# Performance work log

Measured on AMD Instinct MI355X. Metric: run time of the kernel, lower is better.

## Reference

```python
import jax, jax.numpy as jnp
import numpy as np

B, N = 4, 8192
MODEL_DIM, FEAT, HEADS, DIM, SIZE = 512, 64, 8, 3, 32
BN_EPS = 1e-5


def setup_inputs() -> dict:
    key = jax.random.key(0)
    ks = jax.random.split(key, 8)
    return {
        "input": jax.random.normal(ks[0], (B, MODEL_DIM, N), jnp.float32),
        "orig_pcd": jax.random.uniform(ks[1], (B, 3, N), jnp.float32, minval=-1.0, maxval=1.0),
        "conv_w": jax.random.normal(ks[2], (HEADS * (FEAT + 3), MODEL_DIM), jnp.float32) * (MODEL_DIM ** -0.5),
        "key_gamma": jax.random.normal(ks[3], (HEADS * 3,), jnp.float32) * 0.1,
        "key_beta": jnp.zeros((HEADS * 3,), jnp.float32),
        "val_gamma": jnp.ones((HEADS * FEAT,), jnp.float32),
        "val_beta": jnp.zeros((HEADS * FEAT,), jnp.float32),
        "proj": jax.random.normal(ks[4], (HEADS, DIM, 3), jnp.float32) * 0.5,
    }


def _bn(x, gamma, beta):
    # train-mode BatchNorm1d: normalize each channel over (batch, length); x: [B, C, N]
    mu = jnp.mean(x, axis=(0, 2), keepdims=True)
    var = jnp.var(x, axis=(0, 2), keepdims=True)
    xhat = (x - mu) * jax.lax.rsqrt(var + BN_EPS)
    return xhat * gamma[None, :, None] + beta[None, :, None]


def _splat(lattice, values):
    # lattice: [B, H, DIM, N] in (-1, 1); values: [B, H*FEAT, N]
    # DifferentiablePositions: map (-1,1) -> continuous grid coords in [0, SIZE-1]
    c = (lattice + 1.0) * 0.5 * (SIZE - 1)
    f = jnp.clip(jnp.floor(c), 0, SIZE - 2).astype(jnp.int32)   # base corner
    r = c - f.astype(c.dtype)                                    # local coord, [B,H,DIM,N]
    vals = values.reshape(B, HEADS, FEAT, N)
    data = jnp.moveaxis(vals, 2, -1)                             # [B,H,N,FEAT]
    strides = jnp.array([SIZE ** (DIM - 1 - d) for d in range(DIM)], jnp.int32)
    ncells = SIZE ** DIM
    bh = jnp.arange(B)[:, None] * HEADS + jnp.arange(HEADS)[None, :]  # [B,H]
    z = jnp.zeros((B * HEADS * ncells, FEAT), jnp.float32)
    # trilinear splat: scatter-add into the 2^DIM surrounding lattice cells
    for corner in range(2 ** DIM):
        bits = jnp.array([(corner >> (DIM - 1 - d)) & 1 for d in range(DIM)], jnp.int32)
        bits4 = bits[None, None, :, None]
        idx = f + bits4                                           # [B,H,DIM,N]
        w = jnp.prod(jnp.where(bits4 == 1, r, 1.0 - r), axis=2)   # [B,H,N]
        flat = jnp.sum(idx * strides[None, None, :, None], axis=2)  # [B,H,N]
        gid = (bh[:, :, None] * ncells + flat).reshape(-1)        # [B*H*N]
        z = z.at[gid].add((data * w[..., None]).reshape(-1, FEAT))
    return z.reshape(B, HEADS, ncells, FEAT).transpose(0, 1, 3, 2).reshape((B, HEADS, FEAT) + (SIZE,) * DIM)


def reference(input, orig_pcd, conv_w, key_gamma, key_beta, val_gamma, val_beta, proj):
    # 1x1 conv == channel GEMM: [B, H*(FEAT+3), N]
    kv = jnp.einsum('om,bmn->bon', conv_w, input)
    keys_res = _bn(kv[:, :HEADS * 3], key_gamma, key_beta)        # [B, H*3, N]
    values = _bn(kv[:, HEADS * 3:], val_gamma, val_beta)          # [B, H*FEAT, N]
    # per-head learned 3D->DIM projection of (pcd + predicted offset)
    pts = orig_pcd[:, None] + keys_res.reshape(B, HEADS, 3, N)    # [B,H,3,N]
    keys = jnp.einsum('hdk,bhkn->bhdn', proj, pts)                # [B,H,DIM,N]
    lattice = jnp.tanh(keys)
    z = _splat(lattice, values)                                   # [B,H,FEAT,S,S,S]
    occ = (jnp.abs(z) > 1e-9).sum().astype(jnp.float32) / (B * FEAT * HEADS)
    return z, occ, jnp.mean(keys), jnp.var(keys)
```

## Files before the change

kernel.cpp:

```cpp
#include <hip/hip_runtime.h>

#define B_     4
#define N_     8192
#define MD_    512
#define OC_    536
#define HEADS_ 8
#define FEAT_  64
#define NC_    32768
#define ZTOT_  67108864ll
#define NPTS_  262144
#define NKEYS_ 786432.0f

typedef __bf16 bf16x8 __attribute__((ext_vector_type(8)));
typedef float  f32x4  __attribute__((ext_vector_type(4)));

__device__ __forceinline__ unsigned short f2bf(float f) {
  unsigned int u = __float_as_uint(f);
  u = (u + 0x7FFFu + ((u >> 16) & 1u)) >> 16;
  return (unsigned short)u;
}
__device__ __forceinline__ float bf2f(unsigned short s) {
  return __uint_as_float(((unsigned)s) << 16);
}

__global__ __launch_bounds__(256) void convw_kernel(const float* __restrict__ W,
                                                    unsigned short* __restrict__ Wbf) {
  int i = (blockIdx.x * 256 + threadIdx.x) * 4;
  float4 v = *(const float4*)&W[24 * 512 + i];
  ushort4 o;
  o.x = f2bf(v.x); o.y = f2bf(v.y); o.z = f2bf(v.z); o.w = f2bf(v.w);
  *(ushort4*)&Wbf[i] = o;
}

__global__ __launch_bounds__(256) void convxt_kernel(const float* __restrict__ X,
                                                     unsigned short* __restrict__ Xt) {
  const int n0 = blockIdx.x * 64;
  const int k0 = blockIdx.y * 64;
  const int b  = blockIdx.z;
  __shared__ float T[64][65];
  const int t = threadIdx.x;
#pragma unroll
  for (int i = 0; i < 16; ++i) {
    int idx = t + i * 256;
    int kk = idx >> 6, nn = idx & 63;
    T[kk][nn] = X[((size_t)b * MD_ + k0 + kk) * N_ + n0 + nn];
  }
  __syncthreads();
  const int sub = t & 7;
  const int nb  = t >> 3;
#pragma unroll
  for (int i = 0; i < 2; ++i) {
    int nn = nb + i * 32;
    ushort4 o0, o1;
    o0.x = f2bf(T[sub * 8 + 0][nn]); o0.y = f2bf(T[sub * 8 + 1][nn]);
    o0.z = f2bf(T[sub * 8 + 2][nn]); o0.w = f2bf(T[sub * 8 + 3][nn]);
    o1.x = f2bf(T[sub * 8 + 4][nn]); o1.y = f2bf(T[sub * 8 + 5][nn]);
    o1.z = f2bf(T[sub * 8 + 6][nn]); o1.w = f2bf(T[sub * 8 + 7][nn]);
    unsigned short* dst = Xt + ((size_t)b * N_ + n0 + nn) * MD_ + k0 + sub * 8;
    *(ushort4*)dst = o0;
    *(ushort4*)(dst + 4) = o1;
  }
}

__global__ __launch_bounds__(256) void gemm_keys(const float* __restrict__ W,
                                                 const float* __restrict__ X,
                                                 float* __restrict__ kvk,
                                                 float* __restrict__ ssum,
                                                 float* __restrict__ s2sum) {
  const int n0 = blockIdx.x * 256;
  const int b  = blockIdx.y;
  __shared__ float Wt[32][26];
  __shared__ float In[32][260];
  const int t  = threadIdx.x;
  const int cg = t & 63;
  const int rb = (t >> 6) * 6;
  float acc[6][4];
#pragma unroll
  for (int r = 0; r < 6; ++r)
#pragma unroll
    for (int c = 0; c < 4; ++c) acc[r][c] = 0.f;
  const float* Xb = X + (size_t)b * MD_ * N_;
  for (int k0 = 0; k0 < MD_; k0 += 32) {
#pragma unroll
    for (int i = 0; i < 3; ++i) {
      int idx = t * 3 + i;
      int m = idx % 24, k = idx / 24;
      Wt[k][m] = W[(size_t)m * MD_ + k0 + k];
    }
#pragma unroll
    for (int i = 0; i < 8; ++i) {
      int slot = t + i * 256;
      int k = slot >> 6, n4 = slot & 63;
      float4 v = *(const float4*)(Xb + (size_t)(k0 + k) * N_ + n0 + n4 * 4);
      *(float4*)&In[k][n4 * 4] = v;
    }
    __syncthreads();
#pragma unroll
    for (int k = 0; k < 32; ++k) {
      float4 bv = *(const float4*)&In[k][cg * 4];
#pragma unroll
      for (int r = 0; r < 6; ++r) {
        float a = Wt[k][rb + r];
        acc[r][0] = fmaf(a, bv.x, acc[r][0]);
        acc[r][1] = fmaf(a, bv.y, acc[r][1]);
        acc[r][2] = fmaf(a, bv.z, acc[r][2]);
        acc[r][3] = fmaf(a, bv.w, acc[r][3]);
      }
    }
    __syncthreads();
  }
#pragma unroll
  for (int r = 0; r < 6; ++r) {
    float* dst = kvk + ((size_t)b * 24 + rb + r) * N_ + n0 + cg * 4;
    *(float4*)dst = *(float4*)&acc[r][0];
    float s = acc[r][0] + acc[r][1] + acc[r][2] + acc[r][3];
    float s2 = acc[r][0]*acc[r][0] + acc[r][1]*acc[r][1] +
               acc[r][2]*acc[r][2] + acc[r][3]*acc[r][3];
#pragma unroll
    for (int off = 32; off; off >>= 1) {
      s  += __shfl_down(s, off);
      s2 += __shfl_down(s2, off);
    }
    if (cg == 0) { atomicAdd(&ssum[rb + r], s); atomicAdd(&s2sum[rb + r], s2); }
  }
}

__global__ __launch_bounds__(256) void gemm_mfma(const unsigned short* __restrict__ Wbf,
                                                 const unsigned short* __restrict__ Xt,
                                                 unsigned short* __restrict__ valsbf,
                                                 float* __restrict__ ssum,
                                                 float* __restrict__ s2sum) {
  const int m0 = blockIdx.x * 128;
  const int n0 = blockIdx.y * 128;
  const int b  = blockIdx.z;
  __shared__ __align__(16) unsigned short Al[128][72];
  __shared__ __align__(16) unsigned short Bl[128][72];
  const int t = threadIdx.x;
  const int lane = t & 63, wave = t >> 6;
  const int wm = wave >> 1, wn = wave & 1;
  f32x4 acc[4][4];
#pragma unroll
  for (int mi = 0; mi < 4; ++mi)
#pragma unroll
    for (int ni = 0; ni < 4; ++ni)
#pragma unroll
      for (int j = 0; j < 4; ++j) acc[mi][ni][j] = 0.f;

  const unsigned short* Xb = Xt + ((size_t)b * N_ + n0) * MD_;
  for (int k0 = 0; k0 < MD_; k0 += 64) {
#pragma unroll
    for (int i = 0; i < 4; ++i) {
      int chunk = t + i * 256;
      int r = chunk >> 3, c = chunk & 7;
      *(uint4*)&Al[r][c * 8] =
          *(const uint4*)&Wbf[(size_t)(m0 + r) * MD_ + k0 + c * 8];
    }
#pragma unroll
    for (int i = 0; i < 4; ++i) {
      int chunk = t + i * 256;
      int r = chunk >> 3, c = chunk & 7;
      *(uint4*)&Bl[r][c * 8] =
          *(const uint4*)&Xb[(size_t)r * MD_ + k0 + c * 8];
    }
    __syncthreads();
#pragma unroll
    for (int ks = 0; ks < 2; ++ks) {
      bf16x8 af[4], bfr[4];
#pragma unroll
      for (int mi = 0; mi < 4; ++mi)
        af[mi] = *(const bf16x8*)&Al[wm * 64 + mi * 16 + (lane & 15)]
                                    [ks * 32 + (lane >> 4) * 8];
#pragma unroll
      for (int ni = 0; ni < 4; ++ni)
        bfr[ni] = *(const bf16x8*)&Bl[wn * 64 + ni * 16 + (lane & 15)]
                                     [ks * 32 + (lane >> 4) * 8];
#pragma unroll
      for (int mi = 0; mi < 4; ++mi)
#pragma unroll
        for (int ni = 0; ni < 4; ++ni)
          acc[mi][ni] = __builtin_amdgcn_mfma_f32_16x16x32_bf16(
              af[mi], bfr[ni], acc[mi][ni], 0, 0, 0);
    }
    __syncthreads();
  }
#pragma unroll
  for (int mi = 0; mi < 4; ++mi)
#pragma unroll
    for (int j = 0; j < 4; ++j) {
      float s  = acc[mi][0][j] + acc[mi][1][j] + acc[mi][2][j] + acc[mi][3][j];
      float s2 = acc[mi][0][j]*acc[mi][0][j] + acc[mi][1][j]*acc[mi][1][j] +
                 acc[mi][2][j]*acc[mi][2][j] + acc[mi][3][j]*acc[mi][3][j];
#pragma unroll
      for (int off = 1; off < 16; off <<= 1) {
        s  += __shfl_xor(s, off);
        s2 += __shfl_xor(s2, off);
      }
      if ((lane & 15) == 0) {
        int mg = m0 + wm * 64 + mi * 16 + (lane >> 4) * 4 + j;
        atomicAdd(&ssum[24 + mg], s);
        atomicAdd(&s2sum[24 + mg], s2);
      }
    }
#pragma unroll
  for (int mi = 0; mi < 4; ++mi) {
#pragma unroll
    for (int ni = 0; ni < 4; ++ni) {
      int m = m0 + wm * 64 + mi * 16 + (lane >> 4) * 4;
      int n = n0 + wn * 64 + ni * 16 + (lane & 15);
#pragma unroll
      for (int j = 0; j < 4; ++j)
        valsbf[((size_t)b * 512 + m + j) * N_ + n] = f2bf(acc[mi][ni][j]);
    }
  }
}

__global__ __launch_bounds__(256) void bnfin_kernel(const float* __restrict__ ssum,
                                                    const float* __restrict__ s2sum,
                                                    const float* __restrict__ kg,
                                                    const float* __restrict__ kb,
                                                    const float* __restrict__ vg,
                                                    const float* __restrict__ vb,
                                                    float* __restrict__ scale,
                                                    float* __restrict__ shift) {
  const int o = blockIdx.x * 256 + threadIdx.x;
  if (o >= OC_) return;
  const float inv = 1.0f / (B_ * N_);
  float mu  = ssum[o] * inv;
  float var = s2sum[o] * inv - mu * mu;
  float g, be;
  if (o < 24) { g = kg[o]; be = kb[o]; }
  else        { g = vg[o - 24]; be = vb[o - 24]; }
  float sc = g * rsqrtf(var + 1e-5f);
  scale[o] = sc;
  shift[o] = be - mu * sc;
}

__global__ __launch_bounds__(256) void passk_kernel(const float* __restrict__ kvk,
                                                    const float* __restrict__ orig,
                                                    const float* __restrict__ proj,
                                                    const float* __restrict__ scale,
                                                    const float* __restrict__ shift,
                                                    float4* __restrict__ cellr,
                                                    float* __restrict__ kacc) {
  const int p = blockIdx.x * 256 + threadIdx.x;
  const int bh = p >> 13, n = p & (N_ - 1);
  const int b = bh >> 3, h = bh & 7;
  const float* Kb = kvk + (size_t)b * 24 * N_;
  float pt[3];
#pragma unroll
  for (int k = 0; k < 3; ++k) {
    int ch = h * 3 + k;
    float kr = fmaf(Kb[(size_t)ch * N_ + n], scale[ch], shift[ch]);
    pt[k] = orig[((size_t)b * 3 + k) * N_ + n] + kr;
  }
  float ksum = 0.f, ksq = 0.f;
  int cell = 0;
  float rr[3];
#pragma unroll
  for (int d = 0; d < 3; ++d) {
    const float* pr = proj + (h * 3 + d) * 3;
    float key = pr[0] * pt[0] + pr[1] * pt[1] + pr[2] * pt[2];
    ksum += key; ksq += key * key;
    float lat = tanhf(key);
    float c = (lat + 1.0f) * 15.5f;
    float fl = floorf(c);
    fl = fminf(fmaxf(fl, 0.0f), 30.0f);
    rr[d] = c - fl;
    cell += (int)fl * ((d == 0) ? 1024 : (d == 1) ? 32 : 1);
  }
  cellr[p] = make_float4(rr[0], rr[1], rr[2], __int_as_float(cell));
#pragma unroll
  for (int off = 32; off; off >>= 1) {
    ksum += __shfl_down(ksum, off);
    ksq  += __shfl_down(ksq, off);
  }
  if ((threadIdx.x & 63) == 0) {
    atomicAdd(&kacc[0], ksum);
    atomicAdd(&kacc[1], ksq);
  }
}

__global__ __launch_bounds__(1024, 1) void sortk_kernel(const float4* __restrict__ cellr,
                                                        float4* __restrict__ sorted) {
  const int bh = blockIdx.x;
  __shared__ int hist[NC_];
  __shared__ int wsum[16];
  const int t = threadIdx.x;
  for (int i = t; i < NC_; i += 1024) hist[i] = 0;
  __syncthreads();
  const float4* cr = cellr + (size_t)bh * N_;
#pragma unroll
  for (int i = 0; i < 8; ++i) {
    int cell = __float_as_int(cr[t + i * 1024].w);
    atomicAdd(&hist[cell], 1);
  }
  __syncthreads();
  const int base = t * 32;
  int s = 0;
#pragma unroll
  for (int j = 0; j < 32; ++j) s += hist[base + ((j + t) & 31)];
  const int lane = t & 63, wv = t >> 6;
  int sc = s;
#pragma unroll
  for (int off = 1; off < 64; off <<= 1) {
    int x = __shfl_up(sc, off);
    if (lane >= off) sc += x;
  }
  if (lane == 63) wsum[wv] = sc;
  __syncthreads();
  if (t < 16) {
    int x = wsum[t];
    int sc2 = x;
#pragma unroll
    for (int off = 1; off < 16; off <<= 1) {
      int y = __shfl_up(sc2, off);
      if (t >= off) sc2 += y;
    }
    wsum[t] = sc2 - x;
  }
  __syncthreads();
  int run = sc - s + wsum[wv];
#pragma unroll
  for (int j = 0; j < 32; ++j) {
    int idx = base + ((j + t) & 31);
    int v = hist[idx];
    hist[idx] = run;
    run += v;
  }
  __syncthreads();
  float4* dst = sorted + (size_t)bh * N_;
#pragma unroll
  for (int i = 0; i < 8; ++i) {
    int n = t + i * 1024;
    float4 m = cr[n];
    int cell = __float_as_int(m.w);
    int pos = atomicAdd(&hist[cell], 1);
    m.w = __int_as_float(cell | (n << 15));
    dst[pos] = m;
  }
}

__global__ __launch_bounds__(512, 1) void accum_kernel(const unsigned short* __restrict__ valsbf,
                                                       const float* __restrict__ scale,
                                                       const float* __restrict__ shift,
                                                       const float4* __restrict__ sorted,
                                                       float* __restrict__ zout,
                                                       unsigned int* __restrict__ occ) {
  const int blk = blockIdx.x;
  const int f   = blk & 63;
  const int bh  = blk >> 6;
  const int b = bh >> 3, h = bh & 7;
  __shared__ float tile[NC_];
  const int t = threadIdx.x;
#pragma unroll
  for (int i = 0; i < 16; ++i)
    ((float4*)tile)[t + i * 512] = make_float4(0.f, 0.f, 0.f, 0.f);
  __syncthreads();

  const int ch = 24 + h * 64 + f;
  const float sc = scale[ch], sh = shift[ch];
  const unsigned short* kvrow = valsbf + ((size_t)b * 512 + h * 64 + f) * N_;
  const float4* sp = sorted + (size_t)bh * N_;
  const int base = t * 16;

  float4 e[16];
#pragma unroll
  for (int i = 0; i < 16; ++i) e[i] = sp[base + i];
  unsigned short kvv[16];
#pragma unroll
  for (int i = 0; i < 16; ++i)
    kvv[i] = kvrow[((unsigned)__float_as_int(e[i].w)) >> 15];

#define FLUSH8()                                                    \
  {                                                                 \
    atomicAdd(&tile[cur],        m0_);                              \
    atomicAdd(&tile[cur + 1],    m1_);                              \
    atomicAdd(&tile[cur + 32],   m2_);                              \
    atomicAdd(&tile[cur + 33],   m3_);                              \
    atomicAdd(&tile[cur + 1024], m4_);                              \
    atomicAdd(&tile[cur + 1025], m5_);                              \
    atomicAdd(&tile[cur + 1056], m6_);                              \
    atomicAdd(&tile[cur + 1057], m7_);                              \
  }

  float m0_ = 0.f, m1_ = 0.f, m2_ = 0.f, m3_ = 0.f;
  float m4_ = 0.f, m5_ = 0.f, m6_ = 0.f, m7_ = 0.f;
  int cur = __float_as_int(e[0].w) & 32767;
#pragma unroll
  for (int i = 0; i < 16; ++i) {
    int cell = __float_as_int(e[i].w) & 32767;
    if (cell != cur) {
      if (cell == cur + 1) {
        atomicAdd(&tile[cur],        m0_);
        atomicAdd(&tile[cur + 32],   m2_);
        atomicAdd(&tile[cur + 1024], m4_);
        atomicAdd(&tile[cur + 1056], m6_);
        m0_ = m1_; m2_ = m3_; m4_ = m5_; m6_ = m7_;
        m1_ = 0.f; m3_ = 0.f; m5_ = 0.f; m7_ = 0.f;
      } else {
        FLUSH8();
        m0_ = m1_ = m2_ = m3_ = m4_ = m5_ = m6_ = m7_ = 0.f;
      }
      cur = cell;
    }
    float v  = fmaf(bf2f(kvv[i]), sc, sh);
    float r0 = e[i].x, r1 = e[i].y, r2 = e[i].z;
    float va = v * (1.f - r0), vb = v * r0;
    float c00 = (1.f - r1) * (1.f - r2), c01 = (1.f - r1) * r2;
    float c10 = r1 * (1.f - r2),         c11 = r1 * r2;
    m0_ = fmaf(va, c00, m0_); m1_ = fmaf(va, c01, m1_);
    m2_ = fmaf(va, c10, m2_); m3_ = fmaf(va, c11, m3_);
    m4_ = fmaf(vb, c00, m4_); m5_ = fmaf(vb, c01, m5_);
    m6_ = fmaf(vb, c10, m6_); m7_ = fmaf(vb, c11, m7_);
  }
  FLUSH8();
#undef FLUSH8
  __syncthreads();

  unsigned int cnt = 0;
  float* dst = zout + (size_t)blk * NC_;
#pragma unroll
  for (int i = 0; i < 16; ++i) {
    float4 v = ((const float4*)tile)[t + i * 512];
    cnt += (fabsf(v.x) > 1e-9f) ? 1u : 0u;
    cnt += (fabsf(v.y) > 1e-9f) ? 1u : 0u;
    cnt += (fabsf(v.z) > 1e-9f) ? 1u : 0u;
    cnt += (fabsf(v.w) > 1e-9f) ? 1u : 0u;
    ((float4*)dst)[t + i * 512] = v;
  }
#pragma unroll
  for (int off = 32; off; off >>= 1) cnt += __shfl_down(cnt, off);
  __shared__ unsigned int wc[8];
  if ((t & 63) == 0) wc[t >> 6] = cnt;
  __syncthreads();
  if (t == 0) {
    unsigned int s = 0;
#pragma unroll
    for (int i = 0; i < 8; ++i) s += wc[i];
    atomicAdd(occ, s);
  }
}

__global__ __launch_bounds__(256) void gemm_full_kernel(const float* __restrict__ W,
                                                        const float* __restrict__ X,
                                                        float* __restrict__ KV) {
  const int n0 = blockIdx.x * 256;
  const int m0 = blockIdx.y * 64;
  const int b  = blockIdx.z;
  __shared__ float Wt[32][68];
  __shared__ float In[32][260];
  const int t  = threadIdx.x;
  const int tx = t & 31;
  const int ty = t >> 5;
  float acc[8][8];
#pragma unroll
  for (int r = 0; r < 8; ++r)
#pragma unroll
    for (int c = 0; c < 8; ++c) acc[r][c] = 0.f;
  const float* Xb = X + (size_t)b * MD_ * N_;
  for (int k0 = 0; k0 < MD_; k0 += 32) {
#pragma unroll
    for (int i = 0; i < 8; ++i) {
      int idx = t + i * 256;
      int m = idx >> 5, k = idx & 31;
      int mm = m0 + m;
      Wt[k][m] = (mm < OC_) ? W[(size_t)mm * MD_ + (k0 + k)] : 0.f;
    }
#pragma unroll
    for (int i = 0; i < 8; ++i) {
      int slot = t + i * 256;
      int k = slot >> 6, n4 = slot & 63;
      float4 v = *(const float4*)(Xb + (size_t)(k0 + k) * N_ + n0 + n4 * 4);
      *(float4*)&In[k][n4 * 4] = v;
    }
    __syncthreads();
#pragma unroll
    for (int k = 0; k < 32; ++k) {
      float a[8], bb[8];
      *(float4*)&a[0]  = *(const float4*)&Wt[k][ty * 8];
      *(float4*)&a[4]  = *(const float4*)&Wt[k][ty * 8 + 4];
      *(float4*)&bb[0] = *(const float4*)&In[k][tx * 4];
      *(float4*)&bb[4] = *(const float4*)&In[k][128 + tx * 4];
#pragma unroll
      for (int r = 0; r < 8; ++r)
#pragma unroll
        for (int c = 0; c < 8; ++c)
          acc[r][c] = fmaf(a[r], bb[c], acc[r][c]);
    }
    __syncthreads();
  }
#pragma unroll
  for (int r = 0; r < 8; ++r) {
    int mm = m0 + ty * 8 + r;
    if (mm < OC_) {
      float* dst = KV + ((size_t)b * OC_ + mm) * N_ + n0;
      *(float4*)(dst + tx * 4)       = *(float4*)&acc[r][0];
      *(float4*)(dst + 128 + tx * 4) = *(float4*)&acc[r][4];
    }
  }
}

__global__ __launch_bounds__(256) void bn_kernel(const float* __restrict__ KV,
                                                 const float* __restrict__ kg,
                                                 const float* __restrict__ kb,
                                                 const float* __restrict__ vg,
                                                 const float* __restrict__ vb,
                                                 float* __restrict__ scale,
                                                 float* __restrict__ shift) {
  const int o = blockIdx.x;
  const int t = threadIdx.x;
  float s = 0.f, s2 = 0.f;
  for (int idx = t; idx < B_ * N_; idx += 256) {
    int bb = idx >> 13, n = idx & (N_ - 1);
    float v = KV[((size_t)bb * OC_ + o) * N_ + n];
    s += v; s2 = fmaf(v, v, s2);
  }
#pragma unroll
  for (int off = 32; off; off >>= 1) {
    s  += __shfl_down(s, off);
    s2 += __shfl_down(s2, off);
  }
  __shared__ float rs[4], rs2[4];
  if ((t & 63) == 0) { rs[t >> 6] = s; rs2[t >> 6] = s2; }
  __syncthreads();
  if (t == 0) {
    s  = rs[0] + rs[1] + rs[2] + rs[3];
    s2 = rs2[0] + rs2[1] + rs2[2] + rs2[3];
    const float inv = 1.0f / (B_ * N_);
    float mu  = s * inv;
    float var = s2 * inv - mu * mu;
    float g, be;
    if (o < 24) { g = kg[o]; be = kb[o]; }
    else        { g = vg[o - 24]; be = vb[o - 24]; }
    float sc = g * rsqrtf(var + 1e-5f);
    scale[o] = sc;
    shift[o] = be - mu * sc;
  }
}

__global__ __launch_bounds__(256) void splat_final_kernel(const float* __restrict__ KV,
                                                          const float* __restrict__ orig,
                                                          const float* __restrict__ proj,
                                                          const float* __restrict__ scale,
                                                          const float* __restrict__ shift,
                                                          float* __restrict__ Z,
                                                          float* __restrict__ kacc) {
  const int bh = blockIdx.x >> 7;
  const int n0 = (blockIdx.x & 127) << 6;
  const int b = bh >> 3, h = bh & 7;
  __shared__ float vals[64][65];
  __shared__ int   cellS[64];
  __shared__ float rS[64][4];
  const int t = threadIdx.x;
  const float* KVb = KV + (size_t)b * OC_ * N_;
  const int ch0 = 24 + h * 64;
#pragma unroll
  for (int i = 0; i < 16; ++i) {
    int idx = t + i * 256;
    int f = idx >> 6, p = idx & 63;
    int ch = ch0 + f;
    vals[f][p] = fmaf(KVb[(size_t)ch * N_ + n0 + p], scale[ch], shift[ch]);
  }
  if (t < 64) {
    const int n = n0 + t;
    float pt[3];
#pragma unroll
    for (int k = 0; k < 3; ++k) {
      int ch = h * 3 + k;
      float kr = fmaf(KVb[(size_t)ch * N_ + n], scale[ch], shift[ch]);
      pt[k] = orig[((size_t)b * 3 + k) * N_ + n] + kr;
    }
    float ksum = 0.f, ksq = 0.f;
    int cell = 0;
    float rr[3];
#pragma unroll
    for (int d = 0; d < 3; ++d) {
      const float* pr = proj + (h * 3 + d) * 3;
      float key = pr[0] * pt[0] + pr[1] * pt[1] + pr[2] * pt[2];
      ksum += key; ksq += key * key;
      float lat = tanhf(key);
      float c = (lat + 1.0f) * 15.5f;
      float fl = floorf(c);
      fl = fminf(fmaxf(fl, 0.0f), 30.0f);
      rr[d] = c - fl;
      cell += (int)fl * ((d == 0) ? 1024 : (d == 1) ? 32 : 1);
    }
    cellS[t] = cell;
    rS[t][0] = rr[0]; rS[t][1] = rr[1]; rS[t][2] = rr[2];
#pragma unroll
    for (int off = 32; off; off >>= 1) {
      ksum += __shfl_down(ksum, off);
      ksq  += __shfl_down(ksq, off);
    }
    if (t == 0) { atomicAdd(&kacc[0], ksum); atomicAdd(&kacc[1], ksq); }
  }
  __syncthreads();
  const int w = t >> 6, l = t & 63;
  for (int pi = 0; pi < 16; ++pi) {
    int p = w * 16 + pi;
    int cell = cellS[p];
    float r0 = rS[p][0], r1 = rS[p][1], r2 = rS[p][2];
    float u0 = 1.f - r0, u1 = 1.f - r1, u2 = 1.f - r2;
    float v = vals[l][p];
#pragma unroll
    for (int c = 0; c < 8; ++c) {
      float wt = ((c & 4) ? r0 : u0) * ((c & 2) ? r1 : u1) * ((c & 1) ? r2 : u2);
      int cc = cell + ((c & 4) ? 1024 : 0) + ((c & 2) ? 32 : 0) + (c & 1);
      atomicAdd(Z + (size_t)(bh * 64 + l) * NC_ + cc, v * wt);
    }
  }
}

__global__ __launch_bounds__(256) void count_kernel(const float* __restrict__ Z,
                                                    unsigned int* __restrict__ occ) {
  unsigned int cnt = 0;
  for (long long i = (long long)blockIdx.x * blockDim.x + threadIdx.x; i < ZTOT_;
       i += (long long)gridDim.x * blockDim.x)
    cnt += (fabsf(Z[i]) > 1e-9f) ? 1u : 0u;
#pragma unroll
  for (int off = 32; off; off >>= 1) cnt += __shfl_down(cnt, off);
  __shared__ unsigned int wc[4];
  const int t = threadIdx.x;
  if ((t & 63) == 0) wc[t >> 6] = cnt;
  __syncthreads();
  if (t == 0) atomicAdd(occ, wc[0] + wc[1] + wc[2] + wc[3]);
}

__global__ void finalize_kernel(const unsigned int* __restrict__ occ,
                                const float* __restrict__ kacc,
                                float* __restrict__ tail) {
  float mean = kacc[0] / NKEYS_;
  tail[0] = (float)(*occ) * (1.0f / 2048.0f);
  tail[1] = mean;
  tail[2] = kacc[1] / NKEYS_ - mean * mean;
}

extern "C" void kernel_launch(void* const* d_in, const int* in_sizes, int n_in,
                              void* d_out, int out_size, void* d_ws, size_t ws_size,
                              hipStream_t stream) {
  const float* X    = (const float*)d_in[0];
  const float* orig = (const float*)d_in[1];
  const float* W    = (const float*)d_in[2];
  const float* kg   = (const float*)d_in[3];
  const float* kb   = (const float*)d_in[4];
  const float* vg   = (const float*)d_in[5];
  const float* vb   = (const float*)d_in[6];
  const float* proj = (const float*)d_in[7];
  float* out = (float*)d_out;

  float* P = (float*)d_ws;
  float* ssum  = P;
  float* s2sum = P + 544;
  float* kacc  = P + 1088;
  unsigned int* occ = (unsigned int*)(P + 1090);
  float* scale = P + 1152;
  float* shift = P + 1696;
  char* wsb = (char*)d_ws;

  const size_t need = (size_t)60 << 20;
  if (ws_size >= need) {
    unsigned short* Wbf    = (unsigned short*)(wsb + 65536);
    float*          kvk    = (float*)(wsb + ((size_t)1 << 20));
    float4*         sorted = (float4*)(wsb + ((size_t)5 << 20));
    unsigned short* valsbf = (unsigned short*)(wsb + ((size_t)9 << 20));
    unsigned short* Xt = (unsigned short*)out;
    float4* cellr = (float4*)((char*)out + ((size_t)48 << 20));

    hipMemsetAsync(P, 0, 4368, stream);

    convw_kernel<<<256, 256, 0, stream>>>(W, Wbf);
    convxt_kernel<<<dim3(128, 8, 4), 256, 0, stream>>>(X, Xt);
    gemm_keys<<<dim3(32, 4), 256, 0, stream>>>(W, X, kvk, ssum, s2sum);
    gemm_mfma<<<dim3(4, 64, 4), 256, 0, stream>>>(Wbf, Xt, valsbf, ssum, s2sum);
    bnfin_kernel<<<3, 256, 0, stream>>>(ssum, s2sum, kg, kb, vg, vb, scale, shift);
    passk_kernel<<<NPTS_ / 256, 256, 0, stream>>>(kvk, orig, proj, scale, shift,
                                                  cellr, kacc);
    sortk_kernel<<<32, 1024, 0, stream>>>(cellr, sorted);
    accum_kernel<<<2048, 512, 0, stream>>>(valsbf, scale, shift, sorted, out, occ);
    finalize_kernel<<<1, 1, 0, stream>>>(occ, kacc, out + ZTOT_);
  } else {
    float* kv = (float*)(wsb + 16384);
    hipMemsetAsync(P, 0, 4368, stream);
    hipMemsetAsync(out, 0, (size_t)ZTOT_ * 4, stream);
    gemm_full_kernel<<<dim3(N_ / 256, 9, B_), 256, 0, stream>>>(W, X, kv);
    bn_kernel<<<OC_, 256, 0, stream>>>(kv, kg, kb, vg, vb, scale, shift);
    splat_final_kernel<<<B_ * HEADS_ * (N_ / 64), 256, 0, stream>>>(
        kv, orig, proj, scale, shift, out, kacc);
    count_kernel<<<2048, 256, 0, stream>>>(out, occ);
    finalize_kernel<<<1, 1, 0, stream>>>(occ, kacc, out + ZTOT_);
  }
}
```

Measured before the change: 601.7 us.

## Stage GEMM output through LDS for coalesced stores and fold BN finalize into consumers

The MFMA GEMM now writes its bf16 tile into shared memory and then stores full 16-byte rows to global, replacing scattered 2-byte stores. The grid is also reordered so N varies fastest. The separate bnfin kernel is removed, and passk and accum compute BN scale and shift inline from the summed statistics. This saves one launch and improves store coalescing, at the cost of an extra LDS round-trip and some redundant per-thread BN arithmetic.

```diff
diff --git a/kernel.cpp b/kernel.cpp
--- a/kernel.cpp
+++ b/kernel.cpp
@@ -10,6 +10,7 @@
 #define ZTOT_  67108864ll
 #define NPTS_  262144
 #define NKEYS_ 786432.0f
+#define BNINV_ (1.0f / 32768.0f)
 
 typedef __bf16 bf16x8 __attribute__((ext_vector_type(8)));
 typedef float  f32x4  __attribute__((ext_vector_type(4)));
@@ -130,11 +131,13 @@
                                                  unsigned short* __restrict__ valsbf,
                                                  float* __restrict__ ssum,
                                                  float* __restrict__ s2sum) {
-  const int m0 = blockIdx.x * 128;
-  const int n0 = blockIdx.y * 128;
+  const int n0 = blockIdx.x * 128;
+  const int m0 = blockIdx.y * 128;
   const int b  = blockIdx.z;
-  __shared__ __align__(16) unsigned short Al[128][72];
-  __shared__ __align__(16) unsigned short Bl[128][72];
+  __shared__ __align__(16) unsigned short smem[128 * 144];
+#define AL(r, c) smem[(r) * 72 + (c)]
+#define BL(r, c) smem[128 * 72 + (r) * 72 + (c)]
+#define CS(r, c) smem[(r) * 136 + (c)]
   const int t = threadIdx.x;
   const int lane = t & 63, wave = t >> 6;
   const int wm = wave >> 1, wn = wave & 1;
@@ -152,14 +155,14 @@
     for (int i = 0; i < 4; ++i) {
       int chunk = t + i * 256;
       int r = chunk >> 3, c = chunk & 7;
-      *(uint4*)&Al[r][c * 8] =
+      *(uint4*)&AL(r, c * 8) =
           *(const uint4*)&Wbf[(size_t)(m0 + r) * MD_ + k0 + c * 8];
     }
 #pragma unroll
     for (int i = 0; i < 4; ++i) {
       int chunk = t + i * 256;
       int r = chunk >> 3, c = chunk & 7;
-      *(uint4*)&Bl[r][c * 8] =
+      *(uint4*)&BL(r, c * 8) =
           *(const uint4*)&Xb[(size_t)r * MD_ + k0 + c * 8];
     }
     __syncthreads();
@@ -168,12 +171,12 @@
       bf16x8 af[4], bfr[4];
 #pragma unroll
       for (int mi = 0; mi < 4; ++mi)
-        af[mi] = *(const bf16x8*)&Al[wm * 64 + mi * 16 + (lane & 15)]
-                                    [ks * 32 + (lane >> 4) * 8];
+        af[mi] = *(const bf16x8*)&AL(wm * 64 + mi * 16 + (lane & 15),
+                                     ks * 32 + (lane >> 4) * 8);
 #pragma unroll
       for (int ni = 0; ni < 4; ++ni)
-        bfr[ni] = *(const bf16x8*)&Bl[wn * 64 + ni * 16 + (lane & 15)]
-                                     [ks * 32 + (lane >> 4) * 8];
+        bfr[ni] = *(const bf16x8*)&BL(wn * 64 + ni * 16 + (lane & 15),
+                                      ks * 32 + (lane >> 4) * 8);
 #pragma unroll
       for (int mi = 0; mi < 4; ++mi)
 #pragma unroll
@@ -202,44 +205,38 @@
       }
     }
 #pragma unroll
-  for (int mi = 0; mi < 4; ++mi) {
+  for (int mi = 0; mi < 4; ++mi)
 #pragma unroll
     for (int ni = 0; ni < 4; ++ni) {
-      int m = m0 + wm * 64 + mi * 16 + (lane >> 4) * 4;
-      int n = n0 + wn * 64 + ni * 16 + (lane & 15);
+      int row = wm * 64 + mi * 16 + (lane >> 4) * 4;
+      int col = wn * 64 + ni * 16 + (lane & 15);
 #pragma unroll
       for (int j = 0; j < 4; ++j)
-        valsbf[((size_t)b * 512 + m + j) * N_ + n] = f2bf(acc[mi][ni][j]);
-    }
-  }
-}
-
-__global__ __launch_bounds__(256) void bnfin_kernel(const float* __restrict__ ssum,
+        CS(row + j, col) = f2bf(acc[mi][ni][j]);
+    }
+  __syncthreads();
+#pragma unroll
+  for (int i = 0; i < 4; ++i) {
+    int row = (t >> 3) + i * 32;
+    int cb  = (t & 7) * 16;
+    uint4 lo = *(const uint4*)&CS(row, cb);
+    uint4 hi = *(const uint4*)&CS(row, cb + 8);
+    unsigned short* dst = valsbf + ((size_t)b * 512 + m0 + row) * N_ + n0 + cb;
+    *(uint4*)dst       = lo;
+    *(uint4*)(dst + 8) = hi;
+  }
+#undef AL
+#undef BL
+#undef CS
+}
+
+__global__ __launch_bounds__(256) void passk_kernel(const float* __restrict__ kvk,
+                                                    const float* __restrict__ orig,
+                                                    const float* __restrict__ proj,
+                                                    const float* __restrict__ ssum,
                                                     const float* __restrict__ s2sum,
                                                     const float* __restrict__ kg,
                                                     const float* __restrict__ kb,
-                                                    const float* __restrict__ vg,
-                                                    const float* __restrict__ vb,
-                                                    float* __restrict__ scale,
-                                                    float* __restrict__ shift) {
-  const int o = blockIdx.x * 256 + threadIdx.x;
-  if (o >= OC_) return;
-  const float inv = 1.0f / (B_ * N_);
-  float mu  = ssum[o] * inv;
-  float var = s2sum[o] * inv - mu * mu;
-  float g, be;
-  if (o < 24) { g = kg[o]; be = kb[o]; }
-  else        { g = vg[o - 24]; be = vb[o - 24]; }
-  float sc = g * rsqrtf(var + 1e-5f);
-  scale[o] = sc;
-  shift[o] = be - mu * sc;
-}
-
-__global__ __launch_bounds__(256) void passk_kernel(const float* __restrict__ kvk,
-                                                    const float* __restrict__ orig,
-                                                    const float* __restrict__ proj,
-                                                    const float* __restrict__ scale,
-                                                    const float* __restrict__ shift,
                                                     float4* __restrict__ cellr,
                                                     float* __restrict__ kacc) {
   const int p = blockIdx.x * 256 + threadIdx.x;
@@ -250,7 +247,11 @@
 #pragma unroll
   for (int k = 0; k < 3; ++k) {
     int ch = h * 3 + k;
-    float kr = fmaf(Kb[(size_t)ch * N_ + n], scale[ch], shift[ch]);
+    float mu  = ssum[ch] * BNINV_;
+    float var = s2sum[ch] * BNINV_ - mu * mu;
+    float sck = kg[ch] * rsqrtf(var + 1e-5f);
+    float shk = kb[ch] - mu * sck;
+    float kr = fmaf(Kb[(size_t)ch * N_ + n], sck, shk);
     pt[k] = orig[((size_t)b * 3 + k) * N_ + n] + kr;
   }
   float ksum = 0.f, ksq = 0.f;
@@ -341,8 +342,10 @@
 }
 
 __global__ __launch_bounds__(512, 1) void accum_kernel(const unsigned short* __restrict__ valsbf,
-                                                       const float* __restrict__ scale,
-                                                       const float* __restrict__ shift,
+                                                       const float* __restrict__ ssum,
+                                                       const float* __restrict__ s2sum,
+                                                       const float* __restrict__ vg,
+                                                       const float* __restrict__ vb,
                                                        const float4* __restrict__ sorted,
                                                        float* __restrict__ zout,
                                                        unsigned int* __restrict__ occ) {
@@ -358,7 +361,10 @@
   __syncthreads();
 
   const int ch = 24 + h * 64 + f;
-  const float sc = scale[ch], sh = shift[ch];
+  const float mu  = ssum[ch] * BNINV_;
+  const float var = s2sum[ch] * BNINV_ - mu * mu;
+  const float sc  = vg[ch - 24] * rsqrtf(var + 1e-5f);
+  const float sh  = vb[ch - 24] - mu * sc;
   const unsigned short* kvrow = valsbf + ((size_t)b * 512 + h * 64 + f) * N_;
   const float4* sp = sorted + (size_t)bh * N_;
   const int base = t * 16;
@@ -405,13 +411,13 @@
     }
     float v  = fmaf(bf2f(kvv[i]), sc, sh);
     float r0 = e[i].x, r1 = e[i].y, r2 = e[i].z;
-    float va = v * (1.f - r0), vb = v * r0;
+    float va = v * (1.f - r0), vb2 = v * r0;
     float c00 = (1.f - r1) * (1.f - r2), c01 = (1.f - r1) * r2;
     float c10 = r1 * (1.f - r2),         c11 = r1 * r2;
     m0_ = fmaf(va, c00, m0_); m1_ = fmaf(va, c01, m1_);
     m2_ = fmaf(va, c10, m2_); m3_ = fmaf(va, c11, m3_);
-    m4_ = fmaf(vb, c00, m4_); m5_ = fmaf(vb, c01, m5_);
-    m6_ = fmaf(vb, c10, m6_); m7_ = fmaf(vb, c11, m7_);
+    m4_ = fmaf(vb2, c00, m4_); m5_ = fmaf(vb2, c01, m5_);
+    m6_ = fmaf(vb2, c10, m6_); m7_ = fmaf(vb2, c11, m7_);
   }
   FLUSH8();
 #undef FLUSH8
@@ -671,12 +677,12 @@
     convw_kernel<<<256, 256, 0, stream>>>(W, Wbf);
     convxt_kernel<<<dim3(128, 8, 4), 256, 0, stream>>>(X, Xt);
     gemm_keys<<<dim3(32, 4), 256, 0, stream>>>(W, X, kvk, ssum, s2sum);
-    gemm_mfma<<<dim3(4, 64, 4), 256, 0, stream>>>(Wbf, Xt, valsbf, ssum, s2sum);
-    bnfin_kernel<<<3, 256, 0, stream>>>(ssum, s2sum, kg, kb, vg, vb, scale, shift);
-    passk_kernel<<<NPTS_ / 256, 256, 0, stream>>>(kvk, orig, proj, scale, shift,
-                                                  cellr, kacc);
+    gemm_mfma<<<dim3(64, 4, 4), 256, 0, stream>>>(Wbf, Xt, valsbf, ssum, s2sum);
+    passk_kernel<<<NPTS_ / 256, 256, 0, stream>>>(kvk, orig, proj, ssum, s2sum,
+                                                  kg, kb, cellr, kacc);
     sortk_kernel<<<32, 1024, 0, stream>>>(cellr, sorted);
-    accum_kernel<<<2048, 512, 0, stream>>>(valsbf, scale, shift, sorted, out, occ);
+    accum_kernel<<<2048, 512, 0, stream>>>(valsbf, ssum, s2sum, vg, vb,
+                                           sorted, out, occ);
     finalize_kernel<<<1, 1, 0, stream>>>(occ, kacc, out + ZTOT_);
   } else {
     float* kv = (float*)(wsb + 16384);
```

Measured after the change: 593.2 us. About the same (-1.4%).
